# Kernel tuning notes

Measured on AMD Instinct MI355X. Metric: run time of the kernel, lower is better.

Reference implementation:

```python
import jax, jax.numpy as jnp
import numpy as np

N_NODES = 1_000_000
N_EDGES = 16_000_000
BATCH = 1_000_000
EMBED_DIM = 3


def setup_inputs() -> dict:
    key = jax.random.key(0)
    ks = jax.random.split(key, 11)
    edge_index = jax.random.randint(ks[0], (2, N_EDGES), 0, N_NODES, dtype=jnp.int32)
    edge_weight = jax.random.uniform(ks[1], (N_EDGES,), dtype=jnp.float32) + 0.1
    home = jax.random.randint(ks[2], (BATCH,), 0, N_NODES, dtype=jnp.int32)
    away = jax.random.randint(ks[3], (BATCH,), 0, N_NODES, dtype=jnp.int32)
    emb = jax.random.normal(ks[4], (N_NODES, EMBED_DIM), dtype=jnp.float32)
    w_conv = jax.random.normal(ks[5], (3, 3), dtype=jnp.float32) * 0.5
    b_conv = jax.random.normal(ks[6], (3,), dtype=jnp.float32) * 0.1
    w1 = jax.random.normal(ks[7], (6, 6), dtype=jnp.float32) * 0.4
    b1 = jax.random.normal(ks[8], (6,), dtype=jnp.float32) * 0.1
    w3 = jax.random.normal(ks[9], (6, 3), dtype=jnp.float32) * 0.4
    b3 = jax.random.normal(ks[10], (3,), dtype=jnp.float32) * 0.1
    return {"edge_index": edge_index, "edge_weight": edge_weight, "home": home,
            "away": away, "emb": emb, "w_conv": w_conv, "b_conv": b_conv,
            "w1": w1, "b1": b1, "w3": w3, "b3": b3}


def reference(edge_index, edge_weight, home, away, emb, w_conv, b_conv, w1, b1, w3, b3):
    n = emb.shape[0]
    row, col = edge_index[0], edge_index[1]
    # gcn_norm (symmetric, add_self_loops=False): deg over target nodes
    deg = jax.ops.segment_sum(edge_weight, col, num_segments=n)
    dinv = jnp.where(deg > 0, jax.lax.rsqrt(jnp.where(deg > 0, deg, 1.0)), 0.0)
    norm = dinv[row] * edge_weight * dinv[col]  # [E]
    x = emb @ w_conv                            # [N,3] transformed features
    msg = norm[:, None] * x[row]                # [E,3] gather + scale
    agg = jax.ops.segment_sum(msg, col, num_segments=n) + b_conv  # [N,3]
    x = jax.nn.leaky_relu(agg)                  # conv1 output
    h = jnp.concatenate([x[home], x[away]], axis=-1)  # [B,6]
    h = jax.nn.leaky_relu(h @ w1 + b1)          # lin1
    h = jax.nn.leaky_relu(h @ w3 + b3)          # lin3 -> [B,3]
    return jax.nn.log_softmax(h, axis=0)        # LogSoftmax over dim=0 as in source
```

## Files before the change

kernel.cpp:

```cpp
#include <hip/hip_runtime.h>
#include <math.h>

#define NN 1000000
#define NE 16000000
#define NB 1000000
#define NEQ (NE / 4)
#define BN 1024
#define NBUCKA 977
#define NBUCKR 1024
#define NBLK 1024
#define RMASK 0xFFFFFu

#define FPS 512.0f
#define FPINV (1.0f / 512.0f)

typedef int   i32x4 __attribute__((ext_vector_type(4)));
typedef float f32x4 __attribute__((ext_vector_type(4)));

__device__ __forceinline__ float leaky(float v) { return v > 0.f ? v : 0.01f * v; }

#define ATOMF(p, v) unsafeAtomicAdd((p), (v))

__device__ __forceinline__ unsigned int pack_bf32(float x, float y, float z) {
    float m = fmaxf(fmaxf(fabsf(x), fabsf(y)), fabsf(z));
    int ex = ((int)(__float_as_uint(m) >> 23) & 0xFF) - 126;
    ex = min(max(ex, -20), 11);
    float scale = __uint_as_float((unsigned int)(135 - ex) << 23);
    int qx = min(max(__float2int_rn(x * scale), -255), 255);
    int qy = min(max(__float2int_rn(y * scale), -255), 255);
    int qz = min(max(__float2int_rn(z * scale), -255), 255);
    return ((unsigned int)(qx & 0x1FF)) | ((unsigned int)(qy & 0x1FF) << 9) |
           ((unsigned int)(qz & 0x1FF) << 18) | ((unsigned int)(ex + 20) << 27);
}

__device__ __forceinline__ float3 unpack_bf32(unsigned int u) {
    int qx = ((int)(u << 23)) >> 23;
    int qy = ((int)(u << 14)) >> 23;
    int qz = ((int)(u << 5)) >> 23;
    int ex = (int)(u >> 27) - 20;
    float s = __uint_as_float((unsigned int)(ex + 119) << 23);
    return make_float3(qx * s, qy * s, qz * s);
}

__device__ __forceinline__ void atomicMaxF(float* addr, float val) {
    unsigned int* ia = (unsigned int*)addr;
    unsigned int old = *ia;
    while (true) {
        float f = __uint_as_float(old);
        if (f >= val) break;
        unsigned int prev = atomicCAS(ia, old, __float_as_uint(val));
        if (prev == old) break;
        old = prev;
    }
}

__global__ void init_stats(float* stats) {
    int t = threadIdx.x;
    if (t < 3) stats[t] = -1e30f;
    else if (t < 6) stats[t] = 0.f;
}

__global__ __launch_bounds__(256) void count_kernel(const i32x4* __restrict__ col4,
                                                    unsigned int* __restrict__ HG) {
    __shared__ unsigned int h[4][NBUCKR];
    int wave = threadIdx.x >> 6;
    for (int t = threadIdx.x; t < 4 * NBUCKR; t += 256) ((unsigned int*)h)[t] = 0u;
    __syncthreads();
    int stride = gridDim.x * 256;
    for (int i = blockIdx.x * 256 + threadIdx.x; i < NEQ; i += stride) {
        i32x4 c = __builtin_nontemporal_load(col4 + i);
        atomicAdd(&h[wave][((unsigned int)c.x) >> 10], 1u);
        atomicAdd(&h[wave][((unsigned int)c.y) >> 10], 1u);
        atomicAdd(&h[wave][((unsigned int)c.z) >> 10], 1u);
        atomicAdd(&h[wave][((unsigned int)c.w) >> 10], 1u);
    }
    __syncthreads();
    for (int b = threadIdx.x; b < NBUCKR; b += 256)
        HG[(size_t)b * NBLK + blockIdx.x] = h[0][b] + h[1][b] + h[2][b] + h[3][b];
}

__global__ __launch_bounds__(256) void scan_sum(const unsigned int* __restrict__ HG,
                                                unsigned int* __restrict__ part) {
    const unsigned int* p = HG + (size_t)blockIdx.x * NBLK;
    unsigned int s = 0;
    for (int i = threadIdx.x; i < NBLK; i += 256) s += p[i];
    #pragma unroll
    for (int off = 32; off > 0; off >>= 1) s += __shfl_down(s, off);
    __shared__ unsigned int sm[4];
    int wave = threadIdx.x >> 6, lane = threadIdx.x & 63;
    if (lane == 0) sm[wave] = s;
    __syncthreads();
    if (threadIdx.x == 0) part[blockIdx.x] = sm[0] + sm[1] + sm[2] + sm[3];
}

__global__ void scan_part(unsigned int* part) {
    __shared__ unsigned int tmp[256];
    int t = threadIdx.x;
    unsigned int v0 = part[4 * t], v1 = part[4 * t + 1], v2 = part[4 * t + 2], v3 = part[4 * t + 3];
    unsigned int ls = v0 + v1 + v2 + v3;
    tmp[t] = ls;
    __syncthreads();
    for (int off = 1; off < 256; off <<= 1) {
        unsigned int add = (t >= off) ? tmp[t - off] : 0u;
        __syncthreads();
        tmp[t] += add;
        __syncthreads();
    }
    unsigned int base = tmp[t] - ls;
    part[4 * t] = base;
    part[4 * t + 1] = base + v0;
    part[4 * t + 2] = base + v0 + v1;
    part[4 * t + 3] = base + v0 + v1 + v2;
}

__global__ __launch_bounds__(256) void scan_apply(unsigned int* __restrict__ HG,
                                                  const unsigned int* __restrict__ part) {
    __shared__ unsigned int vals[NBLK];
    __shared__ unsigned int ts[256];
    int t = threadIdx.x;
    unsigned int* p = HG + (size_t)blockIdx.x * NBLK;
    for (int i = t; i < NBLK; i += 256) vals[i] = p[i];
    __syncthreads();
    unsigned int a0 = vals[4 * t], a1 = vals[4 * t + 1], a2 = vals[4 * t + 2], a3 = vals[4 * t + 3];
    unsigned int ls = a0 + a1 + a2 + a3;
    ts[t] = ls;
    __syncthreads();
    for (int off = 1; off < 256; off <<= 1) {
        unsigned int add = (t >= off) ? ts[t - off] : 0u;
        __syncthreads();
        ts[t] += add;
        __syncthreads();
    }
    unsigned int base = part[blockIdx.x] + ts[t] - ls;
    p[4 * t] = base;
    p[4 * t + 1] = base + a0;
    p[4 * t + 2] = base + a0 + a1;
    p[4 * t + 3] = base + a0 + a1 + a2;
}

__global__ __launch_bounds__(256) void scatter_kernel(const i32x4* __restrict__ row4,
                                                      const i32x4* __restrict__ col4,
                                                      const f32x4* __restrict__ w4,
                                                      const unsigned int* __restrict__ HG,
                                                      unsigned long long* __restrict__ rec) {
    __shared__ unsigned int pos[NBUCKR];
    for (int b = threadIdx.x; b < NBUCKR; b += 256)
        pos[b] = HG[(size_t)b * NBLK + blockIdx.x];
    __syncthreads();
    int stride = gridDim.x * 256;
    for (int i = blockIdx.x * 256 + threadIdx.x; i < NEQ; i += stride) {
        i32x4 r = __builtin_nontemporal_load(row4 + i);
        i32x4 c = __builtin_nontemporal_load(col4 + i);
        f32x4 w = __builtin_nontemporal_load(w4 + i);
        int rr[4] = {r.x, r.y, r.z, r.w};
        int cc[4] = {c.x, c.y, c.z, c.w};
        float wf[4] = {w.x, w.y, w.z, w.w};
        #pragma unroll
        for (int k = 0; k < 4; k++) {
            unsigned int cu = (unsigned int)cc[k];
            unsigned int p = atomicAdd(&pos[cu >> 10], 1u);
            unsigned long long rk = ((unsigned long long)__float_as_uint(wf[k]) << 32) |
                                    ((cu & 1023u) << 20) | (unsigned int)rr[k];
            rec[p] = rk;
        }
    }
}

__global__ __launch_bounds__(512) void bucket_deg_kernel(const unsigned long long* __restrict__ rec,
                                                         const unsigned int* __restrict__ HG,
                                                         float* __restrict__ deg_g) {
    __shared__ float degl[BN];
    int b = blockIdx.x;
    for (int t = threadIdx.x; t < BN; t += 512) degl[t] = 0.f;
    unsigned int beg = HG[(size_t)b * NBLK];
    unsigned int end = HG[(size_t)(b + 1) * NBLK];
    __syncthreads();
    unsigned int i = beg + threadIdx.x;
    for (; i + 3584 < end; i += 4096) {
        unsigned long long r[8];
        #pragma unroll
        for (int k = 0; k < 8; k++) r[k] = __builtin_nontemporal_load(rec + i + k * 512);
        #pragma unroll
        for (int k = 0; k < 8; k++)
            ATOMF(&degl[(((unsigned int)r[k]) >> 20) & 1023u], __uint_as_float((unsigned int)(r[k] >> 32)));
    }
    for (; i < end; i += 512) {
        unsigned long long r0 = __builtin_nontemporal_load(rec + i);
        ATOMF(&degl[(((unsigned int)r0) >> 20) & 1023u], __uint_as_float((unsigned int)(r0 >> 32)));
    }
    __syncthreads();
    int node0 = b * BN;
    for (int t = threadIdx.x; t < BN; t += 512) {
        int g = node0 + t;
        if (g < NN) deg_g[g] = degl[t];
    }
}

__global__ __launch_bounds__(256) void node1_kernel(const float* __restrict__ deg_g,
                                                    const float* __restrict__ emb,
                                                    const float* __restrict__ w_conv,
                                                    float* __restrict__ dinv,
                                                    unsigned int* __restrict__ y) {
    int g = blockIdx.x * 256 + threadIdx.x;
    if (g >= NN) return;
    float d = deg_g[g];
    float di = d > 0.f ? rsqrtf(d) : 0.f;
    dinv[g] = di;
    float e0 = emb[3 * g], e1 = emb[3 * g + 1], e2 = emb[3 * g + 2];
    float x0 = e0 * w_conv[0] + e1 * w_conv[3] + e2 * w_conv[6];
    float x1 = e0 * w_conv[1] + e1 * w_conv[4] + e2 * w_conv[7];
    float x2 = e0 * w_conv[2] + e1 * w_conv[5] + e2 * w_conv[8];
    y[g] = pack_bf32(di * x0, di * x1, di * x2);
}

__global__ __launch_bounds__(512) void bucket_agg_kernel(const unsigned long long* __restrict__ rec,
                                                         const unsigned int* __restrict__ HG,
                                                         const unsigned int* __restrict__ y,
                                                         unsigned long long* __restrict__ accq) {
    __shared__ unsigned long long accp[BN];
    int b = blockIdx.x;
    for (int t = threadIdx.x; t < BN; t += 512) accp[t] = 0ull;
    unsigned int beg = HG[(size_t)b * NBLK];
    unsigned int end = HG[(size_t)(b + 1) * NBLK];
    __syncthreads();
    unsigned int i = beg + threadIdx.x;
    for (; i + 3584 < end; i += 4096) {
        unsigned long long r[8];
        #pragma unroll
        for (int k = 0; k < 8; k++) r[k] = __builtin_nontemporal_load(rec + i + k * 512);
        unsigned int yu[8];
        #pragma unroll
        for (int k = 0; k < 8; k++) yu[k] = y[((unsigned int)r[k]) & RMASK];
        #pragma unroll
        for (int k = 0; k < 8; k++) {
            float ws = __uint_as_float((unsigned int)(r[k] >> 32)) * FPS;
            float3 yv = unpack_bf32(yu[k]);
            long long q0 = (long long)__float2int_rn(ws * yv.x);
            long long q1 = (long long)__float2int_rn(ws * yv.y);
            long long q2 = (long long)__float2int_rn(ws * yv.z);
            unsigned long long term = (unsigned long long)((q2 << 42) + (q1 << 21) + q0);
            unsigned int c = (((unsigned int)r[k]) >> 20) & 1023u;
            atomicAdd(&accp[c], term);
        }
    }
    for (; i < end; i += 512) {
        unsigned long long r0 = __builtin_nontemporal_load(rec + i);
        float ws = __uint_as_float((unsigned int)(r0 >> 32)) * FPS;
        float3 yv = unpack_bf32(y[((unsigned int)r0) & RMASK]);
        long long q0 = (long long)__float2int_rn(ws * yv.x);
        long long q1 = (long long)__float2int_rn(ws * yv.y);
        long long q2 = (long long)__float2int_rn(ws * yv.z);
        unsigned long long term = (unsigned long long)((q2 << 42) + (q1 << 21) + q0);
        unsigned int c = (((unsigned int)r0) >> 20) & 1023u;
        atomicAdd(&accp[c], term);
    }
    __syncthreads();
    int node0 = b * BN;
    for (int t = threadIdx.x; t < BN; t += 512) {
        int g = node0 + t;
        if (g < NN) accq[g] = accp[t];
    }
}

__global__ __launch_bounds__(256) void node2_kernel(const unsigned long long* __restrict__ accq,
                                                    const float* __restrict__ dinv,
                                                    const float* __restrict__ b_conv,
                                                    unsigned int* __restrict__ xf) {
    int g = blockIdx.x * 256 + threadIdx.x;
    if (g >= NN) return;
    float di = dinv[g];
    long long T = (long long)accq[g];
    long long c0 = (T << 43) >> 43;
    long long T1 = (T - c0) >> 21;
    long long c1 = (T1 << 43) >> 43;
    long long c2 = (T1 - c1) >> 21;
    float a0 = (float)c0 * FPINV;
    float a1 = (float)c1 * FPINV;
    float a2 = (float)c2 * FPINV;
    xf[g] = pack_bf32(leaky(di * a0 + b_conv[0]),
                      leaky(di * a1 + b_conv[1]),
                      leaky(di * a2 + b_conv[2]));
}

__global__ __launch_bounds__(256) void batch_kernel(const i32x4* __restrict__ home4,
                                                    const i32x4* __restrict__ away4,
                                                    const unsigned int* __restrict__ xf,
                                                    const float* __restrict__ w1,
                                                    const float* __restrict__ b1,
                                                    const float* __restrict__ w3,
                                                    const float* __restrict__ b3,
                                                    float4* __restrict__ out4,
                                                    float* __restrict__ stats, int nq) {
    int i = blockIdx.x * blockDim.x + threadIdx.x;
    float m0 = -1e30f, m1 = -1e30f, m2 = -1e30f;
    if (i < nq) {
        float W1[36], B1[6], W3[18], B3[3];
        #pragma unroll
        for (int k = 0; k < 36; k++) W1[k] = w1[k];
        #pragma unroll
        for (int k = 0; k < 6; k++) B1[k] = b1[k];
        #pragma unroll
        for (int k = 0; k < 18; k++) W3[k] = w3[k];
        #pragma unroll
        for (int k = 0; k < 3; k++) B3[k] = b3[k];

        i32x4 hh = __builtin_nontemporal_load(home4 + i);
        i32x4 aa = __builtin_nontemporal_load(away4 + i);
        int hs[4] = {hh.x, hh.y, hh.z, hh.w};
        int as_[4] = {aa.x, aa.y, aa.z, aa.w};
        float o[12];
        #pragma unroll
        for (int e = 0; e < 4; e++) {
            float3 xh = unpack_bf32(xf[hs[e]]);
            float3 xa = unpack_bf32(xf[as_[e]]);
            float h[6] = {xh.x, xh.y, xh.z, xa.x, xa.y, xa.z};
            float l1v[6];
            #pragma unroll
            for (int j = 0; j < 6; j++) {
                float s = B1[j];
                #pragma unroll
                for (int k = 0; k < 6; k++) s += h[k] * W1[k * 6 + j];
                l1v[j] = leaky(s);
            }
            float o3[3];
            #pragma unroll
            for (int j = 0; j < 3; j++) {
                float s = B3[j];
                #pragma unroll
                for (int k = 0; k < 6; k++) s += l1v[k] * W3[k * 3 + j];
                o3[j] = leaky(s);
            }
            o[3 * e + 0] = o3[0];
            o[3 * e + 1] = o3[1];
            o[3 * e + 2] = o3[2];
            m0 = fmaxf(m0, o3[0]);
            m1 = fmaxf(m1, o3[1]);
            m2 = fmaxf(m2, o3[2]);
        }
        #pragma unroll
        for (int q = 0; q < 3; q++)
            out4[3 * (size_t)i + q] = make_float4(o[4 * q], o[4 * q + 1], o[4 * q + 2], o[4 * q + 3]);
    }
    #pragma unroll
    for (int off = 32; off > 0; off >>= 1) {
        m0 = fmaxf(m0, __shfl_down(m0, off));
        m1 = fmaxf(m1, __shfl_down(m1, off));
        m2 = fmaxf(m2, __shfl_down(m2, off));
    }
    __shared__ float sm[3][4];
    int wave = threadIdx.x >> 6, lane = threadIdx.x & 63;
    if (lane == 0) { sm[0][wave] = m0; sm[1][wave] = m1; sm[2][wave] = m2; }
    __syncthreads();
    if (threadIdx.x == 0) {
        atomicMaxF(&stats[0], fmaxf(fmaxf(sm[0][0], sm[0][1]), fmaxf(sm[0][2], sm[0][3])));
        atomicMaxF(&stats[1], fmaxf(fmaxf(sm[1][0], sm[1][1]), fmaxf(sm[1][2], sm[1][3])));
        atomicMaxF(&stats[2], fmaxf(fmaxf(sm[2][0], sm[2][1]), fmaxf(sm[2][2], sm[2][3])));
    }
}

__global__ __launch_bounds__(256) void sumexp_kernel(const float4* __restrict__ out4,
                                                     float* __restrict__ stats, int nq) {
    float mx0 = stats[0], mx1 = stats[1], mx2 = stats[2];
    int i = blockIdx.x * blockDim.x + threadIdx.x;
    float s0 = 0.f, s1 = 0.f, s2 = 0.f;
    if (i < nq) {
        float4 v = out4[i];
        float vals[4] = {v.x, v.y, v.z, v.w};
        int c = (4 * i) % 3;
        #pragma unroll
        for (int e = 0; e < 4; e++) {
            float mv = (c == 0) ? mx0 : ((c == 1) ? mx1 : mx2);
            float ee = expf(vals[e] - mv);
            if (c == 0) s0 += ee; else if (c == 1) s1 += ee; else s2 += ee;
            c = (c == 2) ? 0 : (c + 1);
        }
    }
    #pragma unroll
    for (int off = 32; off > 0; off >>= 1) {
        s0 += __shfl_down(s0, off);
        s1 += __shfl_down(s1, off);
        s2 += __shfl_down(s2, off);
    }
    __shared__ float sm[3][4];
    int wave = threadIdx.x >> 6, lane = threadIdx.x & 63;
    if (lane == 0) { sm[0][wave] = s0; sm[1][wave] = s1; sm[2][wave] = s2; }
    __syncthreads();
    if (threadIdx.x == 0) {
        ATOMF(&stats[3], sm[0][0] + sm[0][1] + sm[0][2] + sm[0][3]);
        ATOMF(&stats[4], sm[1][0] + sm[1][1] + sm[1][2] + sm[1][3]);
        ATOMF(&stats[5], sm[2][0] + sm[2][1] + sm[2][2] + sm[2][3]);
    }
}

__global__ __launch_bounds__(256) void final_kernel(float4* __restrict__ out4,
                                                    const float* __restrict__ stats, int nq) {
    float o0 = stats[0] + logf(stats[3]);
    float o1 = stats[1] + logf(stats[4]);
    float o2 = stats[2] + logf(stats[5]);
    int i = blockIdx.x * blockDim.x + threadIdx.x;
    if (i >= nq) return;
    float4 v = out4[i];
    float vals[4] = {v.x, v.y, v.z, v.w};
    int c = (4 * i) % 3;
    #pragma unroll
    for (int e = 0; e < 4; e++) {
        vals[e] -= (c == 0) ? o0 : ((c == 1) ? o1 : o2);
        c = (c == 2) ? 0 : (c + 1);
    }
    out4[i] = make_float4(vals[0], vals[1], vals[2], vals[3]);
}

extern "C" void kernel_launch(void* const* d_in, const int* in_sizes, int n_in,
                              void* d_out, int out_size, void* d_ws, size_t ws_size,
                              hipStream_t stream) {
    const int*   edge_index  = (const int*)d_in[0];
    const float* edge_weight = (const float*)d_in[1];
    const int*   home        = (const int*)d_in[2];
    const int*   away        = (const int*)d_in[3];
    const float* emb         = (const float*)d_in[4];
    const float* w_conv      = (const float*)d_in[5];
    const float* b_conv      = (const float*)d_in[6];
    const float* w1          = (const float*)d_in[7];
    const float* b1          = (const float*)d_in[8];
    const float* w3          = (const float*)d_in[9];
    const float* b3          = (const float*)d_in[10];
    float* out = (float*)d_out;

    char* ws = (char*)d_ws;
    unsigned long long* rec   = (unsigned long long*)(ws);
    unsigned int*       HG    = (unsigned int*)(ws + 128000000);
    unsigned int*       part  = (unsigned int*)(ws + 132194304);
    float*              deg_g = (float*)(ws + 132198400);
    float*              dinv  = (float*)(ws + 136198400);
    unsigned int*       y     = (unsigned int*)(ws + 140198400);
    unsigned long long* accq  = (unsigned long long*)(ws + 144198400);
    unsigned int*       xf    = (unsigned int*)(ws + 152198400);
    float*              stats = (float*)(ws + 156198400);

    const int* row = edge_index;
    const int* col = edge_index + NE;

    init_stats<<<1, 64, 0, stream>>>(stats);

    count_kernel<<<NBLK, 256, 0, stream>>>((const i32x4*)col, HG);
    scan_sum<<<NBUCKR, 256, 0, stream>>>(HG, part);
    scan_part<<<1, 256, 0, stream>>>(part);
    scan_apply<<<NBUCKR, 256, 0, stream>>>(HG, part);
    scatter_kernel<<<NBLK, 256, 0, stream>>>((const i32x4*)row, (const i32x4*)col,
                                             (const f32x4*)edge_weight, HG, rec);

    bucket_deg_kernel<<<NBUCKA, 512, 0, stream>>>(rec, HG, deg_g);
    node1_kernel<<<(NN + 255) / 256, 256, 0, stream>>>(deg_g, emb, w_conv, dinv, y);
    bucket_agg_kernel<<<NBUCKA, 512, 0, stream>>>(rec, HG, y, accq);
    node2_kernel<<<(NN + 255) / 256, 256, 0, stream>>>(accq, dinv, b_conv, xf);

    const int BQ = NB / 4;
    const int OQ = (NB * 3) / 4;
    batch_kernel<<<(BQ + 255) / 256, 256, 0, stream>>>((const i32x4*)home, (const i32x4*)away, xf,
                                                       w1, b1, w3, b3, (float4*)out, stats, BQ);
    sumexp_kernel<<<(OQ + 255) / 256, 256, 0, stream>>>((const float4*)out, stats, OQ);
    final_kernel<<<(OQ + 255) / 256, 256, 0, stream>>>((float4*)out, stats, OQ);
}
```

Measured before the change: 823.4 us.

## Use coarser 8192-node buckets, compact 6-byte edge records, split bucket work across blocks

Changes the bucket sort from 1024-node to 8192-node buckets (128 buckets). This shrinks the count/scan/scatter histograms and makes scatter writes more coalesced. Edge records shrink from 8 to 6 bytes by quantizing the weight to 12 bits (×2048) packed with the row index, plus a 16-bit local column stored in a separate array. The deg and agg passes split each bucket across 2 and 4 blocks, writing partial results that node1/node2 then sum. The aim is less record traffic and a cheaper scatter, in exchange for weight quantization error and larger shared-memory accumulators (64KB for agg).

Result: no change. 817.0 us (-0.8%).

```diff
diff --git a/kernel.cpp b/kernel.cpp
--- a/kernel.cpp
+++ b/kernel.cpp
@@ -5,11 +5,17 @@
 #define NE 16000000
 #define NB 1000000
 #define NEQ (NE / 4)
-#define BN 1024
-#define NBUCKA 977
-#define NBUCKR 1024
+#define NBUCK2 128
+#define BN2 8192
+#define SH2 13
+#define NBUCKA2 123
+#define DSPLIT 2
+#define ASPLIT 4
 #define NBLK 1024
 #define RMASK 0xFFFFFu
+
+#define W2K 2048.0f
+#define IW2K (1.0f / 2048.0f)
 
 #define FPS 512.0f
 #define FPINV (1.0f / 512.0f)
@@ -62,20 +68,20 @@
 
 __global__ __launch_bounds__(256) void count_kernel(const i32x4* __restrict__ col4,
                                                     unsigned int* __restrict__ HG) {
-    __shared__ unsigned int h[4][NBUCKR];
+    __shared__ unsigned int h[4][NBUCK2];
     int wave = threadIdx.x >> 6;
-    for (int t = threadIdx.x; t < 4 * NBUCKR; t += 256) ((unsigned int*)h)[t] = 0u;
+    for (int t = threadIdx.x; t < 4 * NBUCK2; t += 256) ((unsigned int*)h)[t] = 0u;
     __syncthreads();
     int stride = gridDim.x * 256;
     for (int i = blockIdx.x * 256 + threadIdx.x; i < NEQ; i += stride) {
         i32x4 c = __builtin_nontemporal_load(col4 + i);
-        atomicAdd(&h[wave][((unsigned int)c.x) >> 10], 1u);
-        atomicAdd(&h[wave][((unsigned int)c.y) >> 10], 1u);
-        atomicAdd(&h[wave][((unsigned int)c.z) >> 10], 1u);
-        atomicAdd(&h[wave][((unsigned int)c.w) >> 10], 1u);
-    }
-    __syncthreads();
-    for (int b = threadIdx.x; b < NBUCKR; b += 256)
+        atomicAdd(&h[wave][((unsigned int)c.x) >> SH2], 1u);
+        atomicAdd(&h[wave][((unsigned int)c.y) >> SH2], 1u);
+        atomicAdd(&h[wave][((unsigned int)c.z) >> SH2], 1u);
+        atomicAdd(&h[wave][((unsigned int)c.w) >> SH2], 1u);
+    }
+    __syncthreads();
+    for (int b = threadIdx.x; b < NBUCK2; b += 256)
         HG[(size_t)b * NBLK + blockIdx.x] = h[0][b] + h[1][b] + h[2][b] + h[3][b];
 }
 
@@ -94,23 +100,18 @@
 }
 
 __global__ void scan_part(unsigned int* part) {
-    __shared__ unsigned int tmp[256];
+    __shared__ unsigned int tmp[NBUCK2];
     int t = threadIdx.x;
-    unsigned int v0 = part[4 * t], v1 = part[4 * t + 1], v2 = part[4 * t + 2], v3 = part[4 * t + 3];
-    unsigned int ls = v0 + v1 + v2 + v3;
-    tmp[t] = ls;
-    __syncthreads();
-    for (int off = 1; off < 256; off <<= 1) {
+    unsigned int v = part[t];
+    tmp[t] = v;
+    __syncthreads();
+    for (int off = 1; off < NBUCK2; off <<= 1) {
         unsigned int add = (t >= off) ? tmp[t - off] : 0u;
         __syncthreads();
         tmp[t] += add;
         __syncthreads();
     }
-    unsigned int base = tmp[t] - ls;
-    part[4 * t] = base;
-    part[4 * t + 1] = base + v0;
-    part[4 * t + 2] = base + v0 + v1;
-    part[4 * t + 3] = base + v0 + v1 + v2;
+    part[t] = tmp[t] - v;
 }
 
 __global__ __launch_bounds__(256) void scan_apply(unsigned int* __restrict__ HG,
@@ -142,9 +143,10 @@
                                                       const i32x4* __restrict__ col4,
                                                       const f32x4* __restrict__ w4,
                                                       const unsigned int* __restrict__ HG,
-                                                      unsigned long long* __restrict__ rec) {
-    __shared__ unsigned int pos[NBUCKR];
-    for (int b = threadIdx.x; b < NBUCKR; b += 256)
+                                                      unsigned int* __restrict__ recA,
+                                                      unsigned short* __restrict__ recB) {
+    __shared__ unsigned int pos[NBUCK2];
+    for (int b = threadIdx.x; b < NBUCK2; b += 256)
         pos[b] = HG[(size_t)b * NBLK + blockIdx.x];
     __syncthreads();
     int stride = gridDim.x * 256;
@@ -158,52 +160,62 @@
         #pragma unroll
         for (int k = 0; k < 4; k++) {
             unsigned int cu = (unsigned int)cc[k];
-            unsigned int p = atomicAdd(&pos[cu >> 10], 1u);
-            unsigned long long rk = ((unsigned long long)__float_as_uint(wf[k]) << 32) |
-                                    ((cu & 1023u) << 20) | (unsigned int)rr[k];
-            rec[p] = rk;
+            unsigned int p = atomicAdd(&pos[cu >> SH2], 1u);
+            unsigned int wq = __float2uint_rn(wf[k] * W2K);
+            recA[p] = ((unsigned int)rr[k]) | (wq << 20);
+            recB[p] = (unsigned short)(cu & (BN2 - 1));
         }
     }
 }
 
-__global__ __launch_bounds__(512) void bucket_deg_kernel(const unsigned long long* __restrict__ rec,
+__global__ __launch_bounds__(512) void bucket_deg_kernel(const unsigned int* __restrict__ recA,
+                                                         const unsigned short* __restrict__ recB,
                                                          const unsigned int* __restrict__ HG,
-                                                         float* __restrict__ deg_g) {
-    __shared__ float degl[BN];
-    int b = blockIdx.x;
-    for (int t = threadIdx.x; t < BN; t += 512) degl[t] = 0.f;
-    unsigned int beg = HG[(size_t)b * NBLK];
-    unsigned int end = HG[(size_t)(b + 1) * NBLK];
+                                                         float* __restrict__ deg2) {
+    __shared__ float degl[BN2];
+    int b = blockIdx.x % NBUCKA2;
+    int sp = blockIdx.x / NBUCKA2;
+    for (int t = threadIdx.x; t < BN2; t += 512) degl[t] = 0.f;
+    unsigned int s0 = HG[(size_t)b * NBLK];
+    unsigned int e0 = HG[(size_t)(b + 1) * NBLK];
+    unsigned int n = e0 - s0;
+    unsigned int beg = s0 + (unsigned int)((unsigned long long)n * sp / DSPLIT);
+    unsigned int end = s0 + (unsigned int)((unsigned long long)n * (sp + 1) / DSPLIT);
     __syncthreads();
     unsigned int i = beg + threadIdx.x;
     for (; i + 3584 < end; i += 4096) {
-        unsigned long long r[8];
-        #pragma unroll
-        for (int k = 0; k < 8; k++) r[k] = __builtin_nontemporal_load(rec + i + k * 512);
+        unsigned int a[8];
+        unsigned short bb[8];
+        #pragma unroll
+        for (int k = 0; k < 8; k++) a[k] = __builtin_nontemporal_load(recA + i + k * 512);
+        #pragma unroll
+        for (int k = 0; k < 8; k++) bb[k] = __builtin_nontemporal_load(recB + i + k * 512);
         #pragma unroll
         for (int k = 0; k < 8; k++)
-            ATOMF(&degl[(((unsigned int)r[k]) >> 20) & 1023u], __uint_as_float((unsigned int)(r[k] >> 32)));
+            ATOMF(&degl[bb[k]], (float)(a[k] >> 20) * IW2K);
     }
     for (; i < end; i += 512) {
-        unsigned long long r0 = __builtin_nontemporal_load(rec + i);
-        ATOMF(&degl[(((unsigned int)r0) >> 20) & 1023u], __uint_as_float((unsigned int)(r0 >> 32)));
-    }
-    __syncthreads();
-    int node0 = b * BN;
-    for (int t = threadIdx.x; t < BN; t += 512) {
+        unsigned int a0 = __builtin_nontemporal_load(recA + i);
+        unsigned short b0 = __builtin_nontemporal_load(recB + i);
+        ATOMF(&degl[b0], (float)(a0 >> 20) * IW2K);
+    }
+    __syncthreads();
+    int node0 = b * BN2;
+    float* dst = deg2 + (size_t)sp * NN;
+    for (int t = threadIdx.x; t < BN2; t += 512) {
         int g = node0 + t;
-        if (g < NN) deg_g[g] = degl[t];
-    }
-}
-
-__global__ __launch_bounds__(256) void node1_kernel(const float* __restrict__ deg_g,
+        if (g < NN) dst[g] = degl[t];
+    }
+}
+
+__global__ __launch_bounds__(256) void node1_kernel(const float* __restrict__ deg2,
                                                     const float* __restrict__ emb,
                                                     const float* __restrict__ w_conv,
                                                     float* __restrict__ dinv,
                                                     unsigned int* __restrict__ y) {
     int g = blockIdx.x * 256 + threadIdx.x;
     if (g >= NN) return;
-    float d = deg_g[g];
+    float d = deg2[g] + deg2[NN + g];
     float di = d > 0.f ? rsqrtf(d) : 0.f;
     dinv[g] = di;
     float e0 = emb[3 * g], e1 = emb[3 * g + 1], e2 = emb[3 * g + 2];
@@ -213,52 +225,60 @@
     y[g] = pack_bf32(di * x0, di * x1, di * x2);
 }
 
-__global__ __launch_bounds__(512) void bucket_agg_kernel(const unsigned long long* __restrict__ rec,
+__global__ __launch_bounds__(512) void bucket_agg_kernel(const unsigned int* __restrict__ recA,
+                                                         const unsigned short* __restrict__ recB,
                                                          const unsigned int* __restrict__ HG,
                                                          const unsigned int* __restrict__ y,
                                                          unsigned long long* __restrict__ accq) {
-    __shared__ unsigned long long accp[BN];
-    int b = blockIdx.x;
-    for (int t = threadIdx.x; t < BN; t += 512) accp[t] = 0ull;
-    unsigned int beg = HG[(size_t)b * NBLK];
-    unsigned int end = HG[(size_t)(b + 1) * NBLK];
+    __shared__ unsigned long long accp[BN2];
+    int b = blockIdx.x % NBUCKA2;
+    int sp = blockIdx.x / NBUCKA2;
+    for (int t = threadIdx.x; t < BN2; t += 512) accp[t] = 0ull;
+    unsigned int s0 = HG[(size_t)b * NBLK];
+    unsigned int e0 = HG[(size_t)(b + 1) * NBLK];
+    unsigned int n = e0 - s0;
+    unsigned int beg = s0 + (unsigned int)((unsigned long long)n * sp / ASPLIT);
+    unsigned int end = s0 + (unsigned int)((unsigned long long)n * (sp + 1) / ASPLIT);
     __syncthreads();
     unsigned int i = beg + threadIdx.x;
     for (; i + 3584 < end; i += 4096) {
-        unsigned long long r[8];
-        #pragma unroll
-        for (int k = 0; k < 8; k++) r[k] = __builtin_nontemporal_load(rec + i + k * 512);
+        unsigned int a[8];
+        unsigned short bb[8];
+        #pragma unroll
+        for (int k = 0; k < 8; k++) a[k] = __builtin_nontemporal_load(recA + i + k * 512);
+        #pragma unroll
+        for (int k = 0; k < 8; k++) bb[k] = __builtin_nontemporal_load(recB + i + k * 512);
         unsigned int yu[8];
         #pragma unroll
-        for (int k = 0; k < 8; k++) yu[k] = y[((unsigned int)r[k]) & RMASK];
+        for (int k = 0; k < 8; k++) yu[k] = y[a[k] & RMASK];
         #pragma unroll
         for (int k = 0; k < 8; k++) {
-            float ws = __uint_as_float((unsigned int)(r[k] >> 32)) * FPS;
+            float ws = (float)(a[k] >> 20) * (IW2K * FPS);
             float3 yv = unpack_bf32(yu[k]);
             long long q0 = (long long)__float2int_rn(ws * yv.x);
             long long q1 = (long long)__float2int_rn(ws * yv.y);
             long long q2 = (long long)__float2int_rn(ws * yv.z);
             unsigned long long term = (unsigned long long)((q2 << 42) + (q1 << 21) + q0);
-            unsigned int c = (((unsigned int)r[k]) >> 20) & 1023u;
-            atomicAdd(&accp[c], term);
+            atomicAdd(&accp[bb[k]], term);
         }
     }
     for (; i < end; i += 512) {
-        unsigned long long r0 = __builtin_nontemporal_load(rec + i);
-        float ws = __uint_as_float((unsigned int)(r0 >> 32)) * FPS;
-        float3 yv = unpack_bf32(y[((unsigned int)r0) & RMASK]);
+        unsigned int a0 = __builtin_nontemporal_load(recA + i);
+        unsigned short b0 = __builtin_nontemporal_load(recB + i);
+        float ws = (float)(a0 >> 20) * (IW2K * FPS);
+        float3 yv = unpack_bf32(y[a0 & RMASK]);
         long long q0 = (long long)__float2int_rn(ws * yv.x);
         long long q1 = (long long)__float2int_rn(ws * yv.y);
         long long q2 = (long long)__float2int_rn(ws * yv.z);
         unsigned long long term = (unsigned long long)((q2 << 42) + (q1 << 21) + q0);
-        unsigned int c = (((unsigned int)r0) >> 20) & 1023u;
-        atomicAdd(&accp[c], term);
-    }
-    __syncthreads();
-    int node0 = b * BN;
-    for (int t = threadIdx.x; t < BN; t += 512) {
+        atomicAdd(&accp[b0], term);
+    }
+    __syncthreads();
+    int node0 = b * BN2;
+    unsigned long long* dst = accq + (size_t)sp * NN;
+    for (int t = threadIdx.x; t < BN2; t += 512) {
         int g = node0 + t;
-        if (g < NN) accq[g] = accp[t];
+        if (g < NN) dst[g] = accp[t];
     }
 }
 
@@ -269,14 +289,19 @@
     int g = blockIdx.x * 256 + threadIdx.x;
     if (g >= NN) return;
     float di = dinv[g];
-    long long T = (long long)accq[g];
-    long long c0 = (T << 43) >> 43;
-    long long T1 = (T - c0) >> 21;
-    long long c1 = (T1 << 43) >> 43;
-    long long c2 = (T1 - c1) >> 21;
-    float a0 = (float)c0 * FPINV;
-    float a1 = (float)c1 * FPINV;
-    float a2 = (float)c2 * FPINV;
+    long long s0 = 0, s1 = 0, s2 = 0;
+    #pragma unroll
+    for (int sp = 0; sp < ASPLIT; sp++) {
+        long long T = (long long)accq[(size_t)sp * NN + g];
+        long long c0 = (T << 43) >> 43;
+        long long T1 = (T - c0) >> 21;
+        long long c1 = (T1 << 43) >> 43;
+        long long c2 = (T1 - c1) >> 21;
+        s0 += c0; s1 += c1; s2 += c2;
+    }
+    float a0 = (float)s0 * FPINV;
+    float a1 = (float)s1 * FPINV;
+    float a2 = (float)s2 * FPINV;
     xf[g] = pack_bf32(leaky(di * a0 + b_conv[0]),
                       leaky(di * a1 + b_conv[1]),
                       leaky(di * a2 + b_conv[2]));
@@ -427,15 +452,16 @@
     float* out = (float*)d_out;
 
     char* ws = (char*)d_ws;
-    unsigned long long* rec   = (unsigned long long*)(ws);
-    unsigned int*       HG    = (unsigned int*)(ws + 128000000);
-    unsigned int*       part  = (unsigned int*)(ws + 132194304);
-    float*              deg_g = (float*)(ws + 132198400);
-    float*              dinv  = (float*)(ws + 136198400);
-    unsigned int*       y     = (unsigned int*)(ws + 140198400);
-    unsigned long long* accq  = (unsigned long long*)(ws + 144198400);
-    unsigned int*       xf    = (unsigned int*)(ws + 152198400);
-    float*              stats = (float*)(ws + 156198400);
+    unsigned int*       recA  = (unsigned int*)(ws);
+    unsigned short*     recB  = (unsigned short*)(ws + 64000000);
+    unsigned int*       HG    = (unsigned int*)(ws + 96000000);
+    unsigned int*       part  = (unsigned int*)(ws + 96524288);
+    float*              deg2  = (float*)(ws + 96525312);
+    float*              dinv  = (float*)(ws + 104525312);
+    unsigned int*       y     = (unsigned int*)(ws + 108525312);
+    unsigned long long* accq  = (unsigned long long*)(ws + 112525312);
+    unsigned int*       xf    = (unsigned int*)(ws + 144525312);
+    float*              stats = (float*)(ws + 148525312);
 
     const int* row = edge_index;
     const int* col = edge_index + NE;
@@ -443,15 +469,15 @@
     init_stats<<<1, 64, 0, stream>>>(stats);
 
     count_kernel<<<NBLK, 256, 0, stream>>>((const i32x4*)col, HG);
-    scan_sum<<<NBUCKR, 256, 0, stream>>>(HG, part);
-    scan_part<<<1, 256, 0, stream>>>(part);
-    scan_apply<<<NBUCKR, 256, 0, stream>>>(HG, part);
+    scan_sum<<<NBUCK2, 256, 0, stream>>>(HG, part);
+    scan_part<<<1, NBUCK2, 0, stream>>>(part);
+    scan_apply<<<NBUCK2, 256, 0, stream>>>(HG, part);
     scatter_kernel<<<NBLK, 256, 0, stream>>>((const i32x4*)row, (const i32x4*)col,
-                                             (const f32x4*)edge_weight, HG, rec);
-
-    bucket_deg_kernel<<<NBUCKA, 512, 0, stream>>>(rec, HG, deg_g);
-    node1_kernel<<<(NN + 255) / 256, 256, 0, stream>>>(deg_g, emb, w_conv, dinv, y);
-    bucket_agg_kernel<<<NBUCKA, 512, 0, stream>>>(rec, HG, y, accq);
+                                             (const f32x4*)edge_weight, HG, recA, recB);
+
+    bucket_deg_kernel<<<NBUCKA2 * DSPLIT, 512, 0, stream>>>(recA, recB, HG, deg2);
+    node1_kernel<<<(NN + 255) / 256, 256, 0, stream>>>(deg2, emb, w_conv, dinv, y);
+    bucket_agg_kernel<<<NBUCKA2 * ASPLIT, 512, 0, stream>>>(recA, recB, HG, y, accq);
     node2_kernel<<<(NN + 255) / 256, 256, 0, stream>>>(accq, dinv, b_conv, xf);
 
     const int BQ = NB / 4;
```
